# Optimization experiments

Hardware: AMD Instinct MI355X
Metric: run time of the kernel (lower is better)

The kernel has to match this reference:

```python
import jax, jax.numpy as jnp
import numpy as np

NUM_HEADS = 16
NUM_GROUPS = 4
NUM_KV_HEADS = NUM_HEADS // NUM_GROUPS  # 4
HEAD_DIM = 64
MAX_DIST = 484


def setup_inputs() -> dict:
    key = jax.random.key(0)
    ks = jax.random.split(key, 8)
    B, S, E, H = 32, 484, 1024, 1024
    kv_dim = HEAD_DIM * NUM_GROUPS  # 256
    s_in = 0.03
    return {
        "query": jax.random.normal(ks[0], (B, S, E), dtype=jnp.float32),
        "key": jax.random.normal(ks[1], (B, S, E), dtype=jnp.float32),
        "value": jax.random.normal(ks[2], (B, S, E), dtype=jnp.float32),
        "Wq": jax.random.normal(ks[3], (E, H), dtype=jnp.float32) * s_in,
        "Wk": jax.random.normal(ks[4], (E, kv_dim), dtype=jnp.float32) * s_in,
        "Wv": jax.random.normal(ks[5], (E, kv_dim), dtype=jnp.float32) * s_in,
        "Wo": jax.random.normal(ks[6], (H, E), dtype=jnp.float32) * s_in,
        "rel_table": jax.random.normal(ks[7], (2 * MAX_DIST - 1, NUM_HEADS), dtype=jnp.float32) * 0.02,
    }


def _rel_bias(rel_table, q_len, k_len):
    # relative position k - q, clipped to [-(MD-1), MD-1], shifted to table index
    rel = jnp.arange(k_len)[None, :] - jnp.arange(q_len)[:, None]
    idx = jnp.clip(rel, -(MAX_DIST - 1), MAX_DIST - 1) + (MAX_DIST - 1)
    bias = rel_table[idx]  # [q, k, heads]
    return jnp.transpose(bias, (2, 0, 1))  # [heads, q, k]


def reference(query, key, value, Wq, Wk, Wv, Wo, rel_table):
    B, Q, _ = query.shape
    K = key.shape[1]
    G, Hkv, D = NUM_GROUPS, NUM_KV_HEADS, HEAD_DIM
    # projections; torch head split: head index = g*Hkv + h
    q = (query @ Wq).reshape(B, Q, G * Hkv, D).transpose(0, 2, 1, 3)
    q = q.reshape(B, G, Hkv, Q, D)  # b g h sq d
    k = (key @ Wk).reshape(B, K, G, D).transpose(0, 2, 1, 3)  # b g sk d
    v = (value @ Wv).reshape(B, K, G, D).transpose(0, 2, 1, 3)  # b g sv d
    scale = jnp.float32(D) ** 0.5
    scores = jnp.einsum('bghqd,bgkd->bghqk', q, k) / scale
    bias = _rel_bias(rel_table, Q, K).reshape(1, G, Hkv, Q, K)
    attn = jax.nn.softmax(scores + bias, axis=-1)
    out = jnp.einsum('bghqk,bgkd->bghqd', attn, v)
    out = out.reshape(B, G * Hkv, Q, D).transpose(0, 2, 1, 3).reshape(B, Q, G * Hkv * D)
    return out @ Wo
```

## Files before the change

### kernel.cpp

```cpp
#include <hip/hip_runtime.h>
#include <hip/hip_bf16.h>

typedef __attribute__((ext_vector_type(8))) short short8;
typedef __attribute__((ext_vector_type(4))) float f32x4;
typedef __attribute__((ext_vector_type(4))) unsigned uintx4;

#define B_  32
#define S_  484
#define E_  1024
#define NH  16
#define SP  512
#define M_  (B_*S_)

static __device__ __forceinline__ ushort f2bf(float f) {
  union { float f; unsigned u; } v; v.f = f;
  unsigned u = v.u;
  return (ushort)((u + 0x7FFFu + ((u >> 16) & 1u)) >> 16);
}

static __device__ __forceinline__ unsigned cvt_pk_bf16(float lo, float hi) {
  unsigned r;
  asm("v_cvt_pk_bf16_f32 %0, %1, %2" : "=v"(r) : "v"(lo), "v"(hi));
  return r;
}

#define GLOAD_LDS16(gp, lp) \
  __builtin_amdgcn_global_load_lds((const __attribute__((address_space(1))) void*)(gp), \
                                   (__attribute__((address_space(3))) void*)(lp), 16, 0, 0)

__global__ __launch_bounds__(256)
void cvt_f32_bf16(const float* __restrict__ x, ushort* __restrict__ y, int n4) {
  int i = blockIdx.x * 256 + threadIdx.x;
  int stride = gridDim.x * 256;
  for (; i < n4; i += stride) {
    float4 v = ((const float4*)x)[i];
    ushort4 h;
    h.x = f2bf(v.x); h.y = f2bf(v.y); h.z = f2bf(v.z); h.w = f2bf(v.w);
    ((ushort4*)y)[i] = h;
  }
}

__global__ __launch_bounds__(256)
void transpose_all(const float* __restrict__ Wq, const float* __restrict__ Wk,
                   const float* __restrict__ Wv, const float* __restrict__ Wo,
                   ushort* __restrict__ wqT, ushort* __restrict__ wkT,
                   ushort* __restrict__ wvT, ushort* __restrict__ woT) {
  __shared__ float tile[32][33];
  int t = blockIdx.x;
  const float* W; ushort* WT; int N;
  if (t < 1024)      { W = Wq; WT = wqT; N = 1024; }
  else if (t < 1280) { W = Wk; WT = wkT; N = 256;  t -= 1024; }
  else if (t < 1536) { W = Wv; WT = wvT; N = 256;  t -= 1280; }
  else               { W = Wo; WT = woT; N = 1024; t -= 1536; }
  const int nx = N >> 5;
  const int n0 = (t % nx) * 32, k0 = (t / nx) * 32;
  const int tx = threadIdx.x & 31, ty = threadIdx.x >> 5;
  for (int i = ty; i < 32; i += 8) tile[i][tx] = W[(size_t)(k0 + i) * N + n0 + tx];
  __syncthreads();
  for (int i = ty; i < 32; i += 8) WT[(size_t)(n0 + i) * 1024 + k0 + tx] = f2bf(tile[tx][i]);
}

template<int EPI>
__global__ __launch_bounds__(512)
void gemm_cnt256(const ushort* __restrict__ A, const ushort* __restrict__ BT,
                 void* __restrict__ Cout, float oscale) {
  const int K = 1024, N = 1024, NK = 32;
  __shared__ alignas(16) ushort sA[4][256 * 32];
  __shared__ alignas(16) ushort sB[4][256 * 32];
  const int tid = threadIdx.x;
  const int lane = tid & 63, w = tid >> 6;

  const int nwg = gridDim.x;
  const int qq = nwg >> 3, rr = nwg & 7;
  const int x = blockIdx.x & 7, seq = blockIdx.x >> 3;
  const int logical = x * qq + (x < rr ? x : rr) + seq;
  const int m0 = (logical >> 2) * 256;
  const int n0 = (logical & 3) * 256;

  const int brow = tid >> 2;
  const int scol = (((tid & 3) ^ ((tid >> 3) & 3))) * 8;
  const int rowA0 = min(m0 + brow, M_ - 1);
  const int rowA1 = min(m0 + brow + 128, M_ - 1);
  const ushort* gA0 = A + (size_t)rowA0 * K + scol;
  const ushort* gA1 = A + (size_t)rowA1 * K + scol;
  const ushort* gB0 = BT + (size_t)(n0 + brow) * K + scol;
  const int dst = tid * 8;

  const int wr = w >> 2, wc = w & 3;
  const int g4 = lane >> 4, l16 = lane & 15;
  const int rs = (l16 >> 1) & 3;

  f32x4 acc[8][4] = {};

  auto stage = [&](int kt, int buf) {
    GLOAD_LDS16(gA0 + kt * 32,           &sA[buf][dst]);
    GLOAD_LDS16(gA1 + kt * 32,           &sA[buf][dst + 4096]);
    GLOAD_LDS16(gB0 + kt * 32,           &sB[buf][dst]);
    GLOAD_LDS16(gB0 + kt * 32 + 128 * K, &sB[buf][dst + 4096]);
  };

  stage(0, 0);
  stage(1, 1);
  stage(2, 2);

  int cur = 0;
  for (int kt = 0; kt < NK; ++kt) {
    if (kt < NK - 2)       asm volatile("s_waitcnt vmcnt(8)" ::: "memory");
    else if (kt == NK - 2) asm volatile("s_waitcnt vmcnt(4)" ::: "memory");
    else                   asm volatile("s_waitcnt vmcnt(0)" ::: "memory");
    asm volatile("s_waitcnt lgkmcnt(0)" ::: "memory");
    __builtin_amdgcn_s_barrier();
    if (kt + 3 < NK) stage(kt + 3, (cur + 3) & 3);
    const ushort* pa = &sA[cur][(wr * 128 + l16) * 32 + 8 * (g4 ^ rs)];
    const ushort* pb = &sB[cur][(wc * 64 + l16) * 32 + 8 * (g4 ^ rs)];
    short8 af[8], bf[4];
#pragma unroll
    for (int i = 0; i < 8; ++i) af[i] = *(const short8*)(pa + i * 16 * 32);
#pragma unroll
    for (int i = 0; i < 4; ++i) bf[i] = *(const short8*)(pb + i * 16 * 32);
#pragma unroll
    for (int mi = 0; mi < 8; ++mi)
#pragma unroll
      for (int ni = 0; ni < 4; ++ni)
        acc[mi][ni] = __builtin_amdgcn_mfma_f32_16x16x32_bf16(af[mi], bf[ni], acc[mi][ni], 0, 0, 0);
    cur = (cur + 1) & 3;
  }

#pragma unroll
  for (int mi = 0; mi < 8; ++mi) {
#pragma unroll
    for (int ni = 0; ni < 4; ++ni) {
#pragma unroll
      for (int r = 0; r < 4; ++r) {
        int m = m0 + wr * 128 + mi * 16 + g4 * 4 + r;
        int n = n0 + wc * 64 + ni * 16 + l16;
        if (m < M_) {
          float vv = acc[mi][ni][r];
          if (EPI == 2) {
            ((float*)Cout)[(size_t)m * N + n] = vv;
          } else {
            int b = m / S_, pos = m % S_;
            ushort hv = f2bf(vv * oscale);
            ((ushort*)Cout)[(((size_t)b * NH + (n >> 6)) * SP + pos) * 64 + (n & 63)] = hv;
          }
        }
      }
    }
  }
}

__global__ __launch_bounds__(256)
void kvproj(const float* __restrict__ key, const float* __restrict__ value,
            const ushort* __restrict__ wkT, const ushort* __restrict__ wvT,
            ushort* __restrict__ kp, ushort* __restrict__ vp) {
  const int K = 1024, NK = 32;
  __shared__ alignas(16) ushort sA[2][128 * 32];
  __shared__ alignas(16) ushort sB[2][128 * 32];
  const int tid = threadIdx.x;
  const int lane = tid & 63, w = tid >> 6;

  const int nwg = gridDim.x;
  const int qq = nwg >> 3, rr = nwg & 7;
  const int x = blockIdx.x & 7, seq = blockIdx.x >> 3;
  const int logical = x * qq + (x < rr ? x : rr) + seq;
  const bool isV = logical >= 242;
  const int l2 = isV ? logical - 242 : logical;
  const int m0 = (l2 >> 1) * 128;
  const int n0 = (l2 & 1) * 128;
  const float* Ain = isV ? value : key;
  const ushort* BT = isV ? wvT : wkT;
  ushort* Cout = isV ? vp : kp;

  const int srow = w * 32 + (lane >> 2);
  const int scol = ((lane & 3) ^ ((lane >> 3) & 3)) * 8;
  const ushort* gB0 = BT + (size_t)(n0 + srow) * K + scol;
  const int dstB = srow * 32 + (lane & 3) * 8;

  const int arow = w * 32 + (lane >> 1);
  const int acol = (lane & 1) * 16;
  const int sw = (lane >> 2) & 3;
  const int ag0 = (2 * (lane & 1)) ^ sw;
  const int ag1 = (2 * (lane & 1) + 1) ^ sw;
  const float* gA0f = Ain + (size_t)(m0 + arow) * K + acol;

  const int wr = w >> 1, wc = w & 1;
  const int g4 = lane >> 4, l16 = lane & 15;
  const int rsw = (l16 >> 1) & 3;
  const int aoff = (wr * 64 + l16) * 32 + 8 * (g4 ^ rsw);
  const int boff = (wc * 64 + l16) * 32 + 8 * (g4 ^ rsw);

  f32x4 acc[4][4] = {};
  float4 fA0, fA1, fA2, fA3;

  auto issueA = [&](int kt) {
    const float4* p = (const float4*)(gA0f + kt * 32);
    fA0 = p[0]; fA1 = p[1]; fA2 = p[2]; fA3 = p[3];
  };
  auto writeA = [&](int buf) {
    unsigned d0 = cvt_pk_bf16(fA0.x, fA0.y), d1 = cvt_pk_bf16(fA0.z, fA0.w);
    unsigned d2 = cvt_pk_bf16(fA1.x, fA1.y), d3 = cvt_pk_bf16(fA1.z, fA1.w);
    unsigned d4 = cvt_pk_bf16(fA2.x, fA2.y), d5 = cvt_pk_bf16(fA2.z, fA2.w);
    unsigned d6 = cvt_pk_bf16(fA3.x, fA3.y), d7 = cvt_pk_bf16(fA3.z, fA3.w);
    ushort* base = &sA[buf][arow * 32];
    uintx4 q0 = {d0, d1, d2, d3}, q1 = {d4, d5, d6, d7};
    *(uintx4*)(base + ag0 * 8) = q0;
    *(uintx4*)(base + ag1 * 8) = q1;
  };

  issueA(0);
  GLOAD_LDS16(gB0,          &sB[0][dstB]);
  GLOAD_LDS16(gB0 + 16 * K, &sB[0][dstB + 16 * 32]);
  writeA(0);

  for (int kt = 0; kt < NK; ++kt) {
    __syncthreads();
    const int nb = (kt + 1) & 1;
    if (kt + 1 < NK) {
      const ushort* gb = gB0 + (kt + 1) * 32;
      GLOAD_LDS16(gb,          &sB[nb][dstB]);
      GLOAD_LDS16(gb + 16 * K, &sB[nb][dstB + 16 * 32]);
      issueA(kt + 1);
    }
    const ushort* pa = &sA[kt & 1][aoff];
    const ushort* pb = &sB[kt & 1][boff];
    short8 af[4], bf[4];
#pragma unroll
    for (int i = 0; i < 4; ++i) {
      af[i] = *(const short8*)(pa + i * 16 * 32);
      bf[i] = *(const short8*)(pb + i * 16 * 32);
    }
#pragma unroll
    for (int mi = 0; mi < 4; ++mi)
#pragma unroll
      for (int ni = 0; ni < 4; ++ni)
        acc[mi][ni] = __builtin_amdgcn_mfma_f32_16x16x32_bf16(af[mi], bf[ni], acc[mi][ni], 0, 0, 0);
    if (kt + 1 < NK) writeA(nb);
  }

#pragma unroll
  for (int mi = 0; mi < 4; ++mi) {
#pragma unroll
    for (int ni = 0; ni < 4; ++ni) {
#pragma unroll
      for (int r = 0; r < 4; ++r) {
        int m = m0 + wr * 64 + mi * 16 + g4 * 4 + r;
        int n = n0 + wc * 64 + ni * 16 + l16;
        float vv = acc[mi][ni][r];
        int b = m / S_, pos = m % S_;
        if (!isV) {
          int dd = (n & 63) ^ ((pos & 7) << 3);
          Cout[(((size_t)b * 4 + (n >> 6)) * SP + pos) * 64 + dd] = f2bf(vv);
        } else {
          int local = pos & 31;
          int j = (local < 16) ? (2 * local) : (2 * local - 31);
          int pf_ = (pos & ~31) | (j ^ ((n & 3) << 3));
          Cout[(((size_t)b * 4 + (n >> 6)) * 64 + (n & 63)) * SP + pf_] = f2bf(vv);
        }
      }
    }
  }
}

__global__ __launch_bounds__(256)
void attn_kernel(const ushort* __restrict__ qp, const ushort* __restrict__ kp,
                 const ushort* __restrict__ vpT, const float* __restrict__ rel,
                 ushort* __restrict__ ao) {
  __shared__ float2 sBiasP[1056];
  __shared__ alignas(16) ushort sK[2][32 * 64];
  __shared__ alignas(16) ushort sV[2][64 * 32];
  __shared__ alignas(16) ushort sP[4][16 * 40];
  const int tid = threadIdx.x;
  const int blk = blockIdx.x;
  const int logical = (blk & 7) * 512 + (blk >> 3);
  const int qt = logical & 7, head = (logical >> 3) & 15, b = logical >> 7;
  const int g = head >> 2;
  const float LOG2E = 1.44269504f;
  for (int t = tid; t < 1056; t += 256) {
    float b0 = (t >= 32 && t < 999) ? rel[(t - 32) * 16 + head] * LOG2E : -1e30f;
    int t2 = t + 16;
    float b1 = (t2 >= 32 && t2 < 999) ? rel[(t2 - 32) * 16 + head] * LOG2E : -1e30f;
    sBiasP[t] = make_float2(b0, b1);
  }

  const int lane = tid & 63, w = tid >> 6;
  const int g4 = lane >> 4, l16 = lane & 15;
  const int qw = qt * 64 + w * 16;

  const ushort* qbase = qp + (((size_t)b * NH + head) * SP + qw + l16) * 64;
  short8 qf0 = *(const short8*)(qbase + 8 * g4);
  short8 qf1 = *(const short8*)(qbase + 32 + 8 * g4);

  const ushort* kSrc = kp  + ((size_t)b * 4 + g) * SP * 64 + (tid >> 3) * 64 + (tid & 7) * 8;
  const ushort* vSrc = vpT + ((size_t)b * 4 + g) * 64 * SP + (tid >> 2) * SP + (tid & 3) * 8;

  f32x4 acc[4] = {};
  float ps[4] = {0.f, 0.f, 0.f, 0.f};
  const int ib = l16 - (qw + g4 * 4) + 483 + 32;
  ushort* sPw = &sP[w][0];

  const int kswz  = (l16 & 7) << 3;
  const int kOff0 = l16 * 64 + ((8 * g4) ^ kswz);
  const int kOff1 = l16 * 64 + ((32 + 8 * g4) ^ kswz);
  const int vOff  = l16 * 32 + 8 * (g4 ^ (l16 & 3));

  GLOAD_LDS16(kSrc, &sK[0][w * 512]);
  GLOAD_LDS16(vSrc, &sV[0][w * 512]);

  for (int kt = 0; kt < 16; ++kt) {
    __syncthreads();
    if (kt + 1 < 16) {
      GLOAD_LDS16(kSrc + (kt + 1) * 2048, &sK[(kt + 1) & 1][w * 512]);
      GLOAD_LDS16(vSrc + (kt + 1) * 32,   &sV[(kt + 1) & 1][w * 512]);
    }
    const int k0 = kt * 32;
    float2 bb0 = sBiasP[ib + k0];
    float2 bb1 = sBiasP[ib + k0 - 1];
    float2 bb2 = sBiasP[ib + k0 - 2];
    float2 bb3 = sBiasP[ib + k0 - 3];
    f32x4 s0 = {bb0.x, bb1.x, bb2.x, bb3.x};
    f32x4 s1 = {bb0.y, bb1.y, bb2.y, bb3.y};

    const ushort* sk = &sK[kt & 1][0];
    const ushort* sv = &sV[kt & 1][0];
    short8 kf0 = *(const short8*)(sk + kOff0);
    short8 kf1 = *(const short8*)(sk + kOff1);
    short8 kf2 = *(const short8*)(sk + 1024 + kOff0);
    short8 kf3 = *(const short8*)(sk + 1024 + kOff1);
    __builtin_amdgcn_s_setprio(1);
    s0 = __builtin_amdgcn_mfma_f32_16x16x32_bf16(qf0, kf0, s0, 0, 0, 0);
    s0 = __builtin_amdgcn_mfma_f32_16x16x32_bf16(qf1, kf1, s0, 0, 0, 0);
    s1 = __builtin_amdgcn_mfma_f32_16x16x32_bf16(qf0, kf2, s1, 0, 0, 0);
    s1 = __builtin_amdgcn_mfma_f32_16x16x32_bf16(qf1, kf3, s1, 0, 0, 0);
    __builtin_amdgcn_s_setprio(0);

#pragma unroll
    for (int r = 0; r < 4; ++r) {
      float p0 = __builtin_amdgcn_exp2f(s0[r]);
      float p1 = __builtin_amdgcn_exp2f(s1[r]);
      if (kt == 15) {
        p0 = (k0 + l16 < S_) ? p0 : 0.f;
        p1 = (k0 + 16 + l16 < S_) ? p1 : 0.f;
      }
      ps[r] += p0 + p1;
      *(unsigned*)(sPw + (g4 * 4 + r) * 40 + 2 * l16) = cvt_pk_bf16(p0, p1);
    }
    short8 pf = *(const short8*)(sPw + l16 * 40 + 8 * g4);
    __builtin_amdgcn_s_setprio(1);
#pragma unroll
    for (int nt = 0; nt < 4; ++nt) {
      short8 vf = *(const short8*)(sv + vOff + nt * 512);
      acc[nt] = __builtin_amdgcn_mfma_f32_16x16x32_bf16(pf, vf, acc[nt], 0, 0, 0);
    }
    __builtin_amdgcn_s_setprio(0);
  }

#pragma unroll
  for (int off = 1; off < 16; off <<= 1) {
#pragma unroll
    for (int r = 0; r < 4; ++r) ps[r] += __shfl_xor(ps[r], off, 64);
  }

#pragma unroll
  for (int r = 0; r < 4; ++r) {
    int q_abs = qw + g4 * 4 + r;
    if (q_abs < S_) {
      float inv = 1.f / ps[r];
#pragma unroll
      for (int nt = 0; nt < 4; ++nt) {
        int dd = nt * 16 + l16;
        ao[((size_t)b * S_ + q_abs) * 1024 + head * 64 + dd] = f2bf(acc[nt][r] * inv);
      }
    }
  }
}

extern "C" void kernel_launch(void* const* d_in, const int* in_sizes, int n_in,
                              void* d_out, int out_size, void* d_ws, size_t ws_size,
                              hipStream_t stream) {
  const float* query = (const float*)d_in[0];
  const float* key   = (const float*)d_in[1];
  const float* value = (const float*)d_in[2];
  const float* Wq    = (const float*)d_in[3];
  const float* Wk    = (const float*)d_in[4];
  const float* Wv    = (const float*)d_in[5];
  const float* Wo    = (const float*)d_in[6];
  const float* rel   = (const float*)d_in[7];

  char* ws = (char*)d_ws;
  size_t off = 0;
  auto alloc = [&](size_t bytes) { char* p = ws + off; off += (bytes + 255) & ~(size_t)255; return p; };

  const size_t MEelems = (size_t)M_ * E_;
  ushort* qb  = (ushort*)alloc(MEelems * 2);
  ushort* wqT = (ushort*)alloc((size_t)1024 * 1024 * 2);
  ushort* wkT = (ushort*)alloc((size_t)256 * 1024 * 2);
  ushort* wvT = (ushort*)alloc((size_t)256 * 1024 * 2);
  ushort* woT = (ushort*)alloc((size_t)1024 * 1024 * 2);
  ushort* qp  = (ushort*)alloc((size_t)B_ * NH * SP * 64 * 2);
  ushort* kp  = (ushort*)alloc((size_t)B_ * 4 * SP * 64 * 2);
  ushort* vp  = (ushort*)alloc((size_t)B_ * 4 * 64 * SP * 2);
  ushort* ao  = (ushort*)alloc(MEelems * 2);

  cvt_f32_bf16<<<2048, 256, 0, stream>>>(query, qb, (int)(MEelems / 4));

  transpose_all<<<2560, 256, 0, stream>>>(Wq, Wk, Wv, Wo, wqT, wkT, wvT, woT);

  const float QSCALE = 0.125f * 1.44269504f;
  gemm_cnt256<0><<<244, 512, 0, stream>>>(qb, wqT, qp, QSCALE);
  kvproj<<<484, 256, 0, stream>>>(key, value, wkT, wvT, kp, vp);

  attn_kernel<<<4096, 256, 0, stream>>>(qp, kp, vp, rel, ao);

  gemm_cnt256<2><<<244, 512, 0, stream>>>(ao, woT, d_out, 1.0f);
}
```

Before: 258.4 us.

## Process 32 query rows per wave in attention to reuse K/V tiles

Each wave in the attention kernel now handles two 16-row query tiles, so a block covers 128 queries and the grid is halved. Every K and V fragment loaded from shared memory and every global K/V tile load now serves twice as many MFMAs, cutting LDS and global traffic per unit of work. The s_setprio hints around the MFMA groups are also removed. In exchange, register use and the P buffer in LDS double, which can lower occupancy, and the smaller grid gives less parallelism across CUs.

```diff
diff --git a/kernel.cpp b/kernel.cpp
--- a/kernel.cpp
+++ b/kernel.cpp
@@ -268,11 +268,11 @@
   __shared__ float2 sBiasP[1056];
   __shared__ alignas(16) ushort sK[2][32 * 64];
   __shared__ alignas(16) ushort sV[2][64 * 32];
-  __shared__ alignas(16) ushort sP[4][16 * 40];
+  __shared__ alignas(16) ushort sP[4][32 * 40];
   const int tid = threadIdx.x;
   const int blk = blockIdx.x;
-  const int logical = (blk & 7) * 512 + (blk >> 3);
-  const int qt = logical & 7, head = (logical >> 3) & 15, b = logical >> 7;
+  const int logical = (blk & 7) * 256 + (blk >> 3);
+  const int qt = logical & 3, head = (logical >> 2) & 15, b = logical >> 6;
   const int g = head >> 2;
   const float LOG2E = 1.44269504f;
   for (int t = tid; t < 1056; t += 256) {
@@ -284,18 +284,22 @@
 
   const int lane = tid & 63, w = tid >> 6;
   const int g4 = lane >> 4, l16 = lane & 15;
-  const int qw = qt * 64 + w * 16;
-
-  const ushort* qbase = qp + (((size_t)b * NH + head) * SP + qw + l16) * 64;
-  short8 qf0 = *(const short8*)(qbase + 8 * g4);
-  short8 qf1 = *(const short8*)(qbase + 32 + 8 * g4);
+  const int qw = qt * 128 + w * 32;
+
+  const ushort* qbA = qp + (((size_t)b * NH + head) * SP + qw + l16) * 64;
+  const ushort* qbB = qbA + 16 * 64;
+  short8 qf0a = *(const short8*)(qbA + 8 * g4);
+  short8 qf1a = *(const short8*)(qbA + 32 + 8 * g4);
+  short8 qf0b = *(const short8*)(qbB + 8 * g4);
+  short8 qf1b = *(const short8*)(qbB + 32 + 8 * g4);
 
   const ushort* kSrc = kp  + ((size_t)b * 4 + g) * SP * 64 + (tid >> 3) * 64 + (tid & 7) * 8;
   const ushort* vSrc = vpT + ((size_t)b * 4 + g) * 64 * SP + (tid >> 2) * SP + (tid & 3) * 8;
 
-  f32x4 acc[4] = {};
-  float ps[4] = {0.f, 0.f, 0.f, 0.f};
-  const int ib = l16 - (qw + g4 * 4) + 483 + 32;
+  f32x4 accA[4] = {}, accB[4] = {};
+  float psA[4] = {0.f, 0.f, 0.f, 0.f}, psB[4] = {0.f, 0.f, 0.f, 0.f};
+  const int ibA = l16 - (qw + g4 * 4) + 515;
+  const int ibB = ibA - 16;
   ushort* sPw = &sP[w][0];
 
   const int kswz  = (l16 & 7) << 3;
@@ -313,12 +317,12 @@
       GLOAD_LDS16(vSrc + (kt + 1) * 32,   &sV[(kt + 1) & 1][w * 512]);
     }
     const int k0 = kt * 32;
-    float2 bb0 = sBiasP[ib + k0];
-    float2 bb1 = sBiasP[ib + k0 - 1];
-    float2 bb2 = sBiasP[ib + k0 - 2];
-    float2 bb3 = sBiasP[ib + k0 - 3];
-    f32x4 s0 = {bb0.x, bb1.x, bb2.x, bb3.x};
-    f32x4 s1 = {bb0.y, bb1.y, bb2.y, bb3.y};
+    float2 a0 = sBiasP[ibA + k0],     a1 = sBiasP[ibA + k0 - 1];
+    float2 a2 = sBiasP[ibA + k0 - 2], a3 = sBiasP[ibA + k0 - 3];
+    float2 c0 = sBiasP[ibB + k0],     c1 = sBiasP[ibB + k0 - 1];
+    float2 c2 = sBiasP[ibB + k0 - 2], c3 = sBiasP[ibB + k0 - 3];
+    f32x4 s0a = {a0.x, a1.x, a2.x, a3.x}, s1a = {a0.y, a1.y, a2.y, a3.y};
+    f32x4 s0b = {c0.x, c1.x, c2.x, c3.x}, s1b = {c0.y, c1.y, c2.y, c3.y};
 
     const ushort* sk = &sK[kt & 1][0];
     const ushort* sv = &sV[kt & 1][0];
@@ -326,50 +330,65 @@
     short8 kf1 = *(const short8*)(sk + kOff1);
     short8 kf2 = *(const short8*)(sk + 1024 + kOff0);
     short8 kf3 = *(const short8*)(sk + 1024 + kOff1);
-    __builtin_amdgcn_s_setprio(1);
-    s0 = __builtin_amdgcn_mfma_f32_16x16x32_bf16(qf0, kf0, s0, 0, 0, 0);
-    s0 = __builtin_amdgcn_mfma_f32_16x16x32_bf16(qf1, kf1, s0, 0, 0, 0);
-    s1 = __builtin_amdgcn_mfma_f32_16x16x32_bf16(qf0, kf2, s1, 0, 0, 0);
-    s1 = __builtin_amdgcn_mfma_f32_16x16x32_bf16(qf1, kf3, s1, 0, 0, 0);
-    __builtin_amdgcn_s_setprio(0);
+    s0a = __builtin_amdgcn_mfma_f32_16x16x32_bf16(qf0a, kf0, s0a, 0, 0, 0);
+    s0a = __builtin_amdgcn_mfma_f32_16x16x32_bf16(qf1a, kf1, s0a, 0, 0, 0);
+    s1a = __builtin_amdgcn_mfma_f32_16x16x32_bf16(qf0a, kf2, s1a, 0, 0, 0);
+    s1a = __builtin_amdgcn_mfma_f32_16x16x32_bf16(qf1a, kf3, s1a, 0, 0, 0);
+    s0b = __builtin_amdgcn_mfma_f32_16x16x32_bf16(qf0b, kf0, s0b, 0, 0, 0);
+    s0b = __builtin_amdgcn_mfma_f32_16x16x32_bf16(qf1b, kf1, s0b, 0, 0, 0);
+    s1b = __builtin_amdgcn_mfma_f32_16x16x32_bf16(qf0b, kf2, s1b, 0, 0, 0);
+    s1b = __builtin_amdgcn_mfma_f32_16x16x32_bf16(qf1b, kf3, s1b, 0, 0, 0);
 
 #pragma unroll
     for (int r = 0; r < 4; ++r) {
-      float p0 = __builtin_amdgcn_exp2f(s0[r]);
-      float p1 = __builtin_amdgcn_exp2f(s1[r]);
+      float p0 = __builtin_amdgcn_exp2f(s0a[r]);
+      float p1 = __builtin_amdgcn_exp2f(s1a[r]);
+      float u0 = __builtin_amdgcn_exp2f(s0b[r]);
+      float u1 = __builtin_amdgcn_exp2f(s1b[r]);
       if (kt == 15) {
-        p0 = (k0 + l16 < S_) ? p0 : 0.f;
-        p1 = (k0 + 16 + l16 < S_) ? p1 : 0.f;
+        bool m0v = (k0 + l16 < S_), m1v = (k0 + 16 + l16 < S_);
+        p0 = m0v ? p0 : 0.f;  p1 = m1v ? p1 : 0.f;
+        u0 = m0v ? u0 : 0.f;  u1 = m1v ? u1 : 0.f;
       }
-      ps[r] += p0 + p1;
-      *(unsigned*)(sPw + (g4 * 4 + r) * 40 + 2 * l16) = cvt_pk_bf16(p0, p1);
-    }
-    short8 pf = *(const short8*)(sPw + l16 * 40 + 8 * g4);
-    __builtin_amdgcn_s_setprio(1);
+      psA[r] += p0 + p1;
+      psB[r] += u0 + u1;
+      *(unsigned*)(sPw + (g4 * 4 + r) * 40 + 2 * l16)        = cvt_pk_bf16(p0, p1);
+      *(unsigned*)(sPw + (16 + g4 * 4 + r) * 40 + 2 * l16)   = cvt_pk_bf16(u0, u1);
+    }
+    short8 pfA = *(const short8*)(sPw + l16 * 40 + 8 * g4);
+    short8 pfB = *(const short8*)(sPw + (16 + l16) * 40 + 8 * g4);
 #pragma unroll
     for (int nt = 0; nt < 4; ++nt) {
       short8 vf = *(const short8*)(sv + vOff + nt * 512);
-      acc[nt] = __builtin_amdgcn_mfma_f32_16x16x32_bf16(pf, vf, acc[nt], 0, 0, 0);
-    }
-    __builtin_amdgcn_s_setprio(0);
+      accA[nt] = __builtin_amdgcn_mfma_f32_16x16x32_bf16(pfA, vf, accA[nt], 0, 0, 0);
+      accB[nt] = __builtin_amdgcn_mfma_f32_16x16x32_bf16(pfB, vf, accB[nt], 0, 0, 0);
+    }
   }
 
 #pragma unroll
   for (int off = 1; off < 16; off <<= 1) {
 #pragma unroll
-    for (int r = 0; r < 4; ++r) ps[r] += __shfl_xor(ps[r], off, 64);
+    for (int r = 0; r < 4; ++r) {
+      psA[r] += __shfl_xor(psA[r], off, 64);
+      psB[r] += __shfl_xor(psB[r], off, 64);
+    }
   }
 
 #pragma unroll
   for (int r = 0; r < 4; ++r) {
-    int q_abs = qw + g4 * 4 + r;
-    if (q_abs < S_) {
-      float inv = 1.f / ps[r];
-#pragma unroll
-      for (int nt = 0; nt < 4; ++nt) {
-        int dd = nt * 16 + l16;
-        ao[((size_t)b * S_ + q_abs) * 1024 + head * 64 + dd] = f2bf(acc[nt][r] * inv);
-      }
+    int qa = qw + g4 * 4 + r;
+    if (qa < S_) {
+      float inv = 1.f / psA[r];
+#pragma unroll
+      for (int nt = 0; nt < 4; ++nt)
+        ao[((size_t)b * S_ + qa) * 1024 + head * 64 + nt * 16 + l16] = f2bf(accA[nt][r] * inv);
+    }
+    int qb2 = qa + 16;
+    if (qb2 < S_) {
+      float inv = 1.f / psB[r];
+#pragma unroll
+      for (int nt = 0; nt < 4; ++nt)
+        ao[((size_t)b * S_ + qb2) * 1024 + head * 64 + nt * 16 + l16] = f2bf(accB[nt][r] * inv);
     }
   }
 }
@@ -409,7 +428,7 @@
   gemm_cnt256<0><<<244, 512, 0, stream>>>(qb, wqT, qp, QSCALE);
   kvproj<<<484, 256, 0, stream>>>(key, value, wkT, wvT, kp, vp);
 
-  attn_kernel<<<4096, 256, 0, stream>>>(qp, kp, vp, rel, ao);
+  attn_kernel<<<2048, 256, 0, stream>>>(qp, kp, vp, rel, ao);
 
   gemm_cnt256<2><<<244, 512, 0, stream>>>(ao, woT, d_out, 1.0f);
 }
```

Result: no change. 256.4 us (-0.8%).
